# Kernel tuning notes

Measured on AMD Instinct MI355X. Metric: run time of the kernel, lower is better.

The kernel has to match this reference:

```python
import jax, jax.numpy as jnp
import numpy as np

SEQ, BATCH, IN_DIM, HID = 512, 128, 1024, 1024

def setup_inputs() -> dict:
    key = jax.random.key(0)
    k1, k2, k3, k4 = jax.random.split(key, 4)
    scale = 0.02  # keep gate pre-activations in a sane range
    return {
        "inputs": jax.random.normal(k1, (SEQ, BATCH, IN_DIM), dtype=jnp.float32),
        "proj_W": jax.random.normal(k2, (4 * HID, IN_DIM + HID), dtype=jnp.float32) * scale,
        "proj_b": jax.random.normal(k3, (4 * HID,), dtype=jnp.float32) * scale,
        "qgate_W": jax.random.normal(k4, (HID, HID), dtype=jnp.float32) * scale,
    }

def reference(inputs, proj_W, proj_b, qgate_W):
    # inputs: [S, B, I]; proj_W: [4H, I+H]; qgate_W: [H, H]
    S, B, I = inputs.shape
    H = qgate_W.shape[0]
    Wx = proj_W[:, :I]   # [4H, I]
    Wh = proj_W[:, I:]   # [4H, H]
    # Precompute the input part of proj(cat([x, hx])) for all timesteps (same math).
    x_proj = jnp.einsum('sbi,gi->sbg', inputs, Wx) + proj_b  # [S, B, 4H]

    qWt = qgate_W.T
    def qgate(z):
        return jax.nn.sigmoid(z @ qWt)

    def step(carry, xp):
        hx, cx = carry
        gates = xp + hx @ Wh.T  # [B, 4H]
        f_in, i_in, g_in, o_in = jnp.split(gates, 4, axis=-1)
        # mixed/quantum mode: shared quantum gate, then outer nonlinearity (sigmoid of sigmoid, tanh of sigmoid)
        f = jax.nn.sigmoid(qgate(f_in))
        i = jax.nn.sigmoid(qgate(i_in))
        g = jnp.tanh(qgate(g_in))
        o = jax.nn.sigmoid(qgate(o_in))
        cx = f * cx + i * g
        hx = o * jnp.tanh(cx)
        return (hx, cx), hx

    init = (jnp.zeros((B, H), inputs.dtype), jnp.zeros((B, H), inputs.dtype))
    (hx, cx), outs = jax.lax.scan(step, init, x_proj)
    return outs, hx, cx
```

## Files before the change

kernel.cpp:

```cpp
#include <hip/hip_runtime.h>

typedef unsigned short ushort_t;
typedef __attribute__((ext_vector_type(4))) float f32x4;
typedef __attribute__((ext_vector_type(8))) __bf16 bf16x8;

#define SEQ   512
#define BATCH 128
#define HID   1024
#define G4    4096
#define CHUNK 64
#define BH    (BATCH*HID)
#define NBLK  256
#define FLAG_STRIDE 32
#define SCAN_LDS (131072 + 32768)
#define GEMM256_LDS 131072

__device__ __forceinline__ ushort_t f2bf(float f) {
  unsigned u = __float_as_uint(f);
  u += 0x7FFFu + ((u >> 16) & 1u);
  return (ushort_t)(u >> 16);
}
__device__ __forceinline__ float bf2f(ushort_t h) {
  return __uint_as_float(((unsigned)h) << 16);
}
__device__ __forceinline__ float sigm(float x) { return 1.0f / (1.0f + __expf(-x)); }
__device__ __forceinline__ float ftanh(float x) {
  float xc = fminf(fmaxf(x, -15.f), 15.f);
  float t = __expf(2.f * xc);
  return (t - 1.f) / (t + 1.f);
}

__device__ __forceinline__ void lds16(const ushort_t* g, ushort_t* l) {
  __builtin_amdgcn_global_load_lds(
      (const __attribute__((address_space(1))) unsigned int*)g,
      (__attribute__((address_space(3))) unsigned int*)l, 16, 0, 0);
}
__device__ __forceinline__ void lds16c(const ushort_t* g, ushort_t* l) {
  __builtin_amdgcn_global_load_lds(
      (const __attribute__((address_space(1))) unsigned int*)g,
      (__attribute__((address_space(3))) unsigned int*)l, 16, 0, 0x11);
}

__global__ void cast_f32_bf16(const float* __restrict__ in, ushort_t* __restrict__ out, int n4) {
  int i = blockIdx.x * blockDim.x + threadIdx.x;
  if (i < n4) {
    float4 v = ((const float4*)in)[i];
    union { ushort_t u[4]; uint2 v2; } o;
    o.u[0] = f2bf(v.x); o.u[1] = f2bf(v.y); o.u[2] = f2bf(v.z); o.u[3] = f2bf(v.w);
    ((uint2*)out)[i] = o.v2;
  }
}

__global__ __launch_bounds__(256) void transpose_cast(const float* __restrict__ pw, ushort_t* __restrict__ pwt) {
  __shared__ float tile[32][33];
  int bx = blockIdx.x, by = blockIdx.y;
  int tx = threadIdx.x & 31, ty = threadIdx.x >> 5;
  for (int i = 0; i < 32; i += 8)
    tile[ty + i][tx] = pw[(size_t)(by*32 + ty + i)*2048 + bx*32 + tx];
  __syncthreads();
  for (int i = 0; i < 32; i += 8) {
    int r = ty + i;
    pwt[(size_t)(bx*32 + r)*4096 + by*32 + tx] = f2bf(tile[tx][r]);
  }
}

__global__ void bias_fold(const float* __restrict__ qW, const float* __restrict__ pb, float* __restrict__ b2) {
  int r = blockIdx.x;
  int j = r & (HID-1), gb = r & ~(HID-1);
  float s = 0.f;
  for (int k = threadIdx.x; k < HID; k += 64)
    s += qW[(size_t)j*HID + k] * pb[gb + k];
  for (int off = 32; off; off >>= 1) s += __shfl_down(s, off, 64);
  if (threadIdx.x == 0) b2[r] = s;
}

__global__ __launch_bounds__(256) void gemm128(
    const ushort_t* __restrict__ A, int lda, unsigned arow_mask,
    const ushort_t* __restrict__ B, int ldb, unsigned bko_mask,
    const float* __restrict__ bias, ushort_t* __restrict__ C, int ldc, int K)
{
  __shared__ __align__(16) ushort_t Al[128*64];
  __shared__ __align__(16) ushort_t Bl[128*64];
  const int tid = threadIdx.x, wv = tid >> 6, ln = tid & 63;
  const int bn = blockIdx.x, bm = blockIdx.y;
  const int bko = (int)(((unsigned)(bm << 7)) & bko_mask);
  const int m0 = (wv & 1) << 6, n0 = (wv >> 1) << 6;
  f32x4 acc[4][4] = {};
  for (int k0 = 0; k0 < K; k0 += 64) {
    for (int rr = 0; rr < 4; ++rr) {
      int r0 = (rr << 5) + (wv << 3);
      unsigned ga = ((unsigned)((bm << 7) + r0 + (ln >> 3))) & arow_mask;
      lds16(A + (size_t)ga*lda + k0 + ((ln & 7) << 3), &Al[r0 << 6]);
      unsigned gbr = (unsigned)((bn << 7) + r0 + (ln >> 3));
      lds16(B + (size_t)gbr*ldb + bko + k0 + ((ln & 7) << 3), &Bl[r0 << 6]);
    }
    __syncthreads();
    for (int kk = 0; kk < 64; kk += 32) {
      const int lrow = ln & 15, lk = kk + ((ln >> 4) << 3);
      bf16x8 af[4], bfr[4];
      for (int i = 0; i < 4; ++i) af[i]  = *(const bf16x8*)&Al[((m0 + (i << 4) + lrow) << 6) + lk];
      for (int j = 0; j < 4; ++j) bfr[j] = *(const bf16x8*)&Bl[((n0 + (j << 4) + lrow) << 6) + lk];
      for (int i = 0; i < 4; ++i)
        for (int j = 0; j < 4; ++j)
          acc[i][j] = __builtin_amdgcn_mfma_f32_16x16x32_bf16(af[i], bfr[j], acc[i][j], 0, 0, 0);
    }
    __syncthreads();
  }
  for (int i = 0; i < 4; ++i)
    for (int j = 0; j < 4; ++j) {
      int col = (bn << 7) + n0 + (j << 4) + (ln & 15);
      float bv = bias ? bias[col] : 0.f;
      for (int r = 0; r < 4; ++r) {
        int row = (bm << 7) + m0 + (i << 4) + ((ln >> 4) << 2) + r;
        C[(size_t)row*ldc + col] = f2bf(acc[i][j][r] + bv);
      }
    }
}

__global__ __launch_bounds__(512) void gemm256(
    const ushort_t* __restrict__ A, const ushort_t* __restrict__ B,
    const float* __restrict__ bias, ushort_t* __restrict__ C)
{
  extern __shared__ __align__(16) ushort_t lds[];
  ushort_t* LA = lds;
  ushort_t* LB = lds + 32768;
  const int tid = threadIdx.x, wv8 = tid >> 6, ln = tid & 63;
  const int wm = wv8 >> 2, wn = wv8 & 3;
  const int flat = blockIdx.y * gridDim.x + blockIdx.x;
  const int swz  = ((flat & 7) << 6) | (flat >> 3);
  const int bn = swz & 15, bm = swz >> 4;
  const int lr = ln & 15, lg = ln >> 4;

  f32x4 acc[8][4] = {};
  bf16x8 af[4][2], bfr[4][2];

  auto stA = [&](int db, int half, int kt) {
    ushort_t* d = LA + db*16384 + half*8192 + (wv8 << 9);
    const int ce = ((ln & 7) ^ (ln >> 3)) << 3;
    #pragma unroll
    for (int p = 0; p < 2; ++p) {
      int rr = half*128 + p*64 + (wv8 << 3) + (ln >> 3);
      lds16(A + (size_t)(bm*256 + rr)*1024 + kt*64 + ce, d + p*4096);
    }
  };
  auto stB = [&](int db, int half, int kt) {
    ushort_t* d = LB + db*16384 + half*8192 + (wv8 << 9);
    const int ce = ((ln & 7) ^ (ln >> 3)) << 3;
    #pragma unroll
    for (int p = 0; p < 2; ++p) {
      int rr = half*128 + p*64 + (wv8 << 3) + (ln >> 3);
      lds16(B + (size_t)(bn*256 + rr)*2048 + kt*64 + ce, d + p*4096);
    }
  };

#define RD_A(DB, MQ) { _Pragma("unroll") for (int i_ = 0; i_ < 4; ++i_) { \
    const int row_ = ((MQ)*4 + i_)*16 + lr; \
    const ushort_t* b_ = &LA[(DB)*16384 + wm*8192 + row_*64]; \
    af[i_][0] = *(const bf16x8*)&b_[ (lg << 3)       ^ ((lr & 7) << 3)]; \
    af[i_][1] = *(const bf16x8*)&b_[((lg << 3) | 32) ^ ((lr & 7) << 3)]; } }

#define RD_B(DB, NQ) { _Pragma("unroll") for (int j_ = 0; j_ < 2; ++j_) { \
    const int row_ = (wn & 1)*64 + ((NQ)*2 + j_)*16 + lr; \
    const ushort_t* b_ = &LB[(DB)*16384 + (wn >> 1)*8192 + row_*64]; \
    bfr[(NQ)*2 + j_][0] = *(const bf16x8*)&b_[ (lg << 3)       ^ ((lr & 7) << 3)]; \
    bfr[(NQ)*2 + j_][1] = *(const bf16x8*)&b_[((lg << 3) | 32) ^ ((lr & 7) << 3)]; } }

#define QUAD(MQ, NQ) \
  __builtin_amdgcn_s_setprio(1); \
  { _Pragma("unroll") for (int i_ = 0; i_ < 4; ++i_) \
      _Pragma("unroll") for (int j_ = 0; j_ < 2; ++j_) \
        _Pragma("unroll") for (int k_ = 0; k_ < 2; ++k_) \
          acc[(MQ)*4 + i_][(NQ)*2 + j_] = __builtin_amdgcn_mfma_f32_16x16x32_bf16( \
              af[i_][k_], bfr[(NQ)*2 + j_][k_], acc[(MQ)*4 + i_][(NQ)*2 + j_], 0, 0, 0); } \
  __builtin_amdgcn_s_setprio(0);

#define BAR() __builtin_amdgcn_s_barrier()
#define LGK0() do { asm volatile("s_waitcnt lgkmcnt(0)" ::: "memory"); \
                    __builtin_amdgcn_sched_barrier(0); } while (0)
#define VM4() do { asm volatile("s_waitcnt vmcnt(4)" ::: "memory"); \
                   __builtin_amdgcn_sched_barrier(0); } while (0)

  stA(0,0,0); stA(0,1,0); stB(0,0,0); stB(0,1,0); stB(1,0,1); stB(1,1,1);
  asm volatile("s_waitcnt vmcnt(4)" ::: "memory");
  BAR();

  for (int i = 0; i < 8; ++i) {
    const int k1 = 2*i + 1, k2 = 2*i + 2, k3 = 2*i + 3;
    RD_A(0,0); RD_B(0,0); stA(1,0,k1);            BAR(); LGK0(); QUAD(0,0); BAR();
    RD_B(0,1); stA(1,1,k1);                       BAR(); LGK0(); QUAD(0,1); BAR();
    RD_A(0,1); if (k2 < 16) stB(0,0,k2);          BAR(); LGK0(); QUAD(1,0); BAR();
    if (k2 < 16) stB(0,1,k2);                     BAR();         QUAD(1,1); VM4(); BAR();
    RD_A(1,0); RD_B(1,0); if (k2 < 16) stA(0,0,k2); BAR(); LGK0(); QUAD(0,0); BAR();
    RD_B(1,1); if (k2 < 16) stA(0,1,k2);          BAR(); LGK0(); QUAD(0,1); BAR();
    RD_A(1,1); if (k3 < 16) stB(1,0,k3);          BAR(); LGK0(); QUAD(1,0); BAR();
    if (k3 < 16) stB(1,1,k3);                     BAR();         QUAD(1,1); VM4(); BAR();
  }

  const int crow0 = bm*256 + wm*128;
  const int ccol0 = bn*256 + wn*64;
  #pragma unroll
  for (int m = 0; m < 8; ++m)
    #pragma unroll
    for (int n = 0; n < 4; ++n) {
      int col = ccol0 + n*16 + lr;
      float bv = bias[col];
      #pragma unroll
      for (int r = 0; r < 4; ++r) {
        int row = crow0 + m*16 + lg*4 + r;
        C[(size_t)row*4096 + col] = f2bf(acc[m][n][r] + bv);
      }
    }
#undef RD_A
#undef RD_B
#undef QUAD
#undef BAR
#undef LGK0
#undef VM4
}

__global__ __launch_bounds__(256, 1) void qlstm_scan(
    const ushort_t* __restrict__ P,
    const ushort_t* __restrict__ W2,
    ushort_t* __restrict__ hxb,
    float* __restrict__ cxg,
    float* __restrict__ outc,
    int t0,
    unsigned* __restrict__ flags)
{
  extern __shared__ __align__(16) ushort_t lds[];
  ushort_t* Ul = lds;
  ushort_t* Ar = lds + 65536;
  float*    sm = (float*)(lds + 65536);

  const int tid = threadIdx.x, wv = tid >> 6, ln = tid & 63;
  const int rblk = blockIdx.x & 3, cblk = blockIdx.x >> 2;
  unsigned* gflags = flags + (size_t)rblk*64*FLAG_STRIDE;

  for (int ck = 0; ck < 8; ++ck)
    for (int rr = 0; rr < 4; ++rr) {
      int lr = rr*16 + wv*4 + (ln >> 4);
      int grow = ((lr >> 4) << 10) + cblk*16 + (lr & 15);
      int gcol = ck*128 + (((ln & 15) ^ (lr & 7)) << 3);
      lds16(W2 + (size_t)grow*2048 + 1024 + gcol, &Ul[ck*8192 + (rr*16 + wv*4)*128]);
    }

  const int b_loc = tid >> 3;
  const int j0    = (tid & 7) << 1;
  const size_t ci = (size_t)(rblk*32 + b_loc)*1024 + cblk*16 + j0;
  float2 cxr = *(const float2*)&cxg[ci];

  auto stageA = [&](int slot, int k0, const ushort_t* hxR) {
    #pragma unroll
    for (int rr = 0; rr < 2; ++rr) {
      int row = rr*16 + wv*4 + (ln >> 4);
      int gcol = ((ln & 15) ^ (row & 7)) << 3;
      lds16c(hxR + (size_t)(rblk*32 + row)*1024 + k0 + gcol,
             &Ar[slot*4096 + (rr*16 + wv*4)*128]);
    }
  };
  auto load_pv = [&](int tl, float* pv) {
    #pragma unroll
    for (int i = 0; i < 2; ++i)
      #pragma unroll
      for (int r = 0; r < 4; ++r) {
        int bl = i*16 + ((ln >> 4) << 2) + r;
        pv[i*4+r] = bf2f(P[(size_t)(tl*128 + rblk*32 + bl)*4096 + (wv << 10) + cblk*16 + (ln & 15)]);
      }
  };

  float pv[8];
  load_pv(0, pv);

  for (int tl = 0; tl < CHUNK; ++tl) {
    const int t = t0 + tl;
    const ushort_t* hxR = hxb + (size_t)(t % 3)*BH;
    ushort_t*       hxW = hxb + (size_t)((t + 1) % 3)*BH;

    f32x4 acc0 = {}, acc1 = {};
    stageA(0, 0, hxR);
    stageA(1, 128, hxR);
    stageA(2, 256, hxR);

    #define COMPUTE_CK(CK)                                                         \
      {                                                                            \
        const int aslot = (CK) & 3;                                                \
        _Pragma("unroll")                                                          \
        for (int k4 = 0; k4 < 4; ++k4) {                                           \
          int s = k4*4 + (ln >> 4);                                                \
          int ar0 = ln & 15, ar1 = 16 + (ln & 15);                                 \
          int brow = wv*16 + (ln & 15);                                            \
          bf16x8 a0 = *(const bf16x8*)&Ar[aslot*4096 + ar0*128 + ((s ^ (ar0 & 7)) << 3)]; \
          bf16x8 a1 = *(const bf16x8*)&Ar[aslot*4096 + ar1*128 + ((s ^ (ar1 & 7)) << 3)]; \
          bf16x8 bb = *(const bf16x8*)&Ul[(CK)*8192 + brow*128 + ((s ^ (brow & 7)) << 3)]; \
          acc0 = __builtin_amdgcn_mfma_f32_16x16x32_bf16(a0, bb, acc0, 0, 0, 0);   \
          acc1 = __builtin_amdgcn_mfma_f32_16x16x32_bf16(a1, bb, acc1, 0, 0, 0);   \
        }                                                                          \
      }
    #define STEP_CK(CK, WN, DOSTAGE)                                               \
      asm volatile("s_waitcnt vmcnt(" #WN ")" ::: "memory");                       \
      __builtin_amdgcn_s_barrier();                                                \
      if (DOSTAGE) stageA(((CK)+3) & 3, ((CK)+3)*128, hxR);                        \
      COMPUTE_CK(CK)

    STEP_CK(0, 4, 1) STEP_CK(1, 4, 1) STEP_CK(2, 4, 1)
    STEP_CK(3, 4, 1) STEP_CK(4, 4, 1)
    STEP_CK(5, 4, 0) STEP_CK(6, 2, 0) STEP_CK(7, 0, 0)
    #undef STEP_CK
    #undef COMPUTE_CK

    #pragma unroll
    for (int i = 0; i < 2; ++i)
      #pragma unroll
      for (int r = 0; r < 4; ++r) {
        int bl = i*16 + ((ln >> 4) << 2) + r;
        float v = (i ? acc1[r] : acc0[r]) + pv[i*4+r];
        sm[wv*512 + bl*16 + (ln & 15)] = sigm(v);
      }
    __syncthreads();
    float2 h2;
    {
      const float2* sm2 = (const float2*)sm;
      int e = b_loc*8 + (j0 >> 1);
      float2 sF = sm2[0*256 + e], sI = sm2[1*256 + e];
      float2 sG = sm2[2*256 + e], sO = sm2[3*256 + e];
      float f0 = sigm(sF.x), i0 = sigm(sI.x), g0 = ftanh(sG.x), o0 = sigm(sO.x);
      float f1 = sigm(sF.y), i1 = sigm(sI.y), g1 = ftanh(sG.y), o1 = sigm(sO.y);
      float cn0 = f0*cxr.x + i0*g0, cn1 = f1*cxr.y + i1*g1;
      float h0 = o0*ftanh(cn0),     h1 = o1*ftanh(cn1);
      cxr.x = cn0; cxr.y = cn1;
      h2.x = h0; h2.y = h1;
      unsigned hp = (unsigned)f2bf(h0) | ((unsigned)f2bf(h1) << 16);
      __hip_atomic_store((unsigned*)&hxW[ci], hp,
                         __ATOMIC_RELAXED, __HIP_MEMORY_SCOPE_AGENT);
    }

    if (tl != CHUNK - 1) {
      const unsigned gen = (unsigned)(t + 1);
      asm volatile("s_waitcnt vmcnt(0)" ::: "memory");
      __syncthreads();
      if (tid == 0)
        __hip_atomic_store(gflags + (size_t)cblk*FLAG_STRIDE, gen,
                           __ATOMIC_RELAXED, __HIP_MEMORY_SCOPE_AGENT);
      *(float2*)&outc[(size_t)tl*BH + ci] = h2;
      float pvn[8];
      load_pv(tl + 1, pvn);
      if (tid < 64) {
        int it = 0;
        for (;;) {
          unsigned a = __hip_atomic_load(gflags + (size_t)tid*FLAG_STRIDE,
                                         __ATOMIC_RELAXED, __HIP_MEMORY_SCOPE_AGENT);
          if (__all(a >= gen)) break;
          if ((++it & 255) == 0) __builtin_amdgcn_fence(__ATOMIC_ACQUIRE, "agent");
          __builtin_amdgcn_s_sleep(1);
        }
      }
      __syncthreads();
      #pragma unroll
      for (int q = 0; q < 8; ++q) pv[q] = pvn[q];
    } else {
      *(float2*)&outc[(size_t)tl*BH + ci] = h2;
    }
  }
  *(float2*)&cxg[ci] = cxr;
}

extern "C" void kernel_launch(void* const* d_in, const int* in_sizes, int n_in,
                              void* d_out, int out_size, void* d_ws, size_t ws_size,
                              hipStream_t stream) {
  const float* x  = (const float*)d_in[0];
  const float* pW = (const float*)d_in[1];
  const float* pb = (const float*)d_in[2];
  const float* qW = (const float*)d_in[3];
  float* out = (float*)d_out;

  char* w = (char*)d_ws;
  auto carve = [&](size_t bytes) { char* p = w; w += (bytes + 255) & ~(size_t)255; return p; };
  ushort_t* qWbf = (ushort_t*)carve((size_t)HID*HID*2);
  ushort_t* pWt  = (ushort_t*)carve((size_t)2048*4096*2);
  ushort_t* W2   = (ushort_t*)carve((size_t)4096*2048*2);
  float*    b2   = (float*)   carve((size_t)4096*4);
  ushort_t* hxb  = (ushort_t*)carve((size_t)3*BH*2);
  float*    cxws = (float*)   carve((size_t)BH*4);
  unsigned* flags= (unsigned*)carve((size_t)NBLK*FLAG_STRIDE*4);
  ushort_t* xbf  = (ushort_t*)carve((size_t)CHUNK*BATCH*HID*2);
  ushort_t* Pc   = (ushort_t*)carve((size_t)CHUNK*BATCH*G4*2);

  (void)hipFuncSetAttribute((const void*)qlstm_scan,
                            hipFuncAttributeMaxDynamicSharedMemorySize, SCAN_LDS);
  (void)hipFuncSetAttribute((const void*)gemm256,
                            hipFuncAttributeMaxDynamicSharedMemorySize, GEMM256_LDS);

  cast_f32_bf16<<<(HID*HID/4 + 255)/256, 256, 0, stream>>>(qW, qWbf, HID*HID/4);
  transpose_cast<<<dim3(64, 128), 256, 0, stream>>>(pW, pWt);
  bias_fold<<<4096, 64, 0, stream>>>(qW, pb, b2);
  gemm128<<<dim3(16, 32), 256, 0, stream>>>(qWbf, 1024, 1023u, pWt, 4096, ~1023u, nullptr, W2, 2048, 1024);

  hipMemsetAsync(hxb, 0, (size_t)BH*2, stream);
  hipMemsetAsync(cxws, 0, (size_t)BH*4, stream);
  hipMemsetAsync(flags, 0, (size_t)NBLK*FLAG_STRIDE*4, stream);

  for (int c = 0; c < SEQ/CHUNK; ++c) {
    cast_f32_bf16<<<(CHUNK*BATCH*HID/4 + 255)/256, 256, 0, stream>>>(
        x + (size_t)c*CHUNK*BATCH*HID, xbf, CHUNK*BATCH*HID/4);
    gemm256<<<dim3(G4/256, CHUNK*BATCH/256), 512, GEMM256_LDS, stream>>>(
        xbf, W2, b2, Pc);

    const ushort_t* Pa = Pc; const ushort_t* W2a = W2;
    ushort_t* hxa = hxb; float* cxa = cxws;
    float* outa = out + (size_t)c*CHUNK*BH;
    int t0 = c*CHUNK; unsigned* fla = flags;
    void* args[7] = { &Pa, &W2a, &hxa, &cxa, &outa, &t0, &fla };
    hipLaunchCooperativeKernel((const void*)qlstm_scan, dim3(NBLK), dim3(256),
                               args, SCAN_LDS, stream);
  }
  hipMemcpyAsync(out + (size_t)SEQ*BH,      out + (size_t)(SEQ-1)*BH, (size_t)BH*4,
                 hipMemcpyDeviceToDevice, stream);
  hipMemcpyAsync(out + (size_t)SEQ*BH + BH, cxws, (size_t)BH*4,
                 hipMemcpyDeviceToDevice, stream);
}
```

Measured before the change: 2.981 ms.

## Replace flag barrier with generation-tagged hidden-state words polled per chunk

Removes the per-step global flag barrier between scan blocks. Each hidden-state pair is now stored as a 64-bit word tagged with its generation number. Consumers poll the tagged words for each K-chunk directly and spin until all eight words match the expected generation, then unpack them into LDS. This lets a block start computing on early chunks while other producers are still finishing, and it removes the vmcnt drain and flag store. In exchange, hidden-state traffic doubles, LDS staging moves from async global-to-LDS loads to register loads plus LDS writes, and every step spins on many addresses.

```diff
diff --git a/kernel.cpp b/kernel.cpp
--- a/kernel.cpp
+++ b/kernel.cpp
@@ -1,6 +1,7 @@
 #include <hip/hip_runtime.h>
 
 typedef unsigned short ushort_t;
+typedef unsigned long long u64;
 typedef __attribute__((ext_vector_type(4))) float f32x4;
 typedef __attribute__((ext_vector_type(8))) __bf16 bf16x8;
 
@@ -11,9 +12,9 @@
 #define CHUNK 64
 #define BH    (BATCH*HID)
 #define NBLK  256
-#define FLAG_STRIDE 32
 #define SCAN_LDS (131072 + 32768)
 #define GEMM256_LDS 131072
+#define HXATOMS 65536
 
 __device__ __forceinline__ ushort_t f2bf(float f) {
   unsigned u = __float_as_uint(f);
@@ -34,11 +35,6 @@
   __builtin_amdgcn_global_load_lds(
       (const __attribute__((address_space(1))) unsigned int*)g,
       (__attribute__((address_space(3))) unsigned int*)l, 16, 0, 0);
-}
-__device__ __forceinline__ void lds16c(const ushort_t* g, ushort_t* l) {
-  __builtin_amdgcn_global_load_lds(
-      (const __attribute__((address_space(1))) unsigned int*)g,
-      (__attribute__((address_space(3))) unsigned int*)l, 16, 0, 0x11);
 }
 
 __global__ void cast_f32_bf16(const float* __restrict__ in, ushort_t* __restrict__ out, int n4) {
@@ -221,11 +217,10 @@
 __global__ __launch_bounds__(256, 1) void qlstm_scan(
     const ushort_t* __restrict__ P,
     const ushort_t* __restrict__ W2,
-    ushort_t* __restrict__ hxb,
+    u64* __restrict__ hx2,
     float* __restrict__ cxg,
     float* __restrict__ outc,
-    int t0,
-    unsigned* __restrict__ flags)
+    int t0)
 {
   extern __shared__ __align__(16) ushort_t lds[];
   ushort_t* Ul = lds;
@@ -234,30 +229,31 @@
 
   const int tid = threadIdx.x, wv = tid >> 6, ln = tid & 63;
   const int rblk = blockIdx.x & 3, cblk = blockIdx.x >> 2;
-  unsigned* gflags = flags + (size_t)rblk*64*FLAG_STRIDE;
 
   for (int ck = 0; ck < 8; ++ck)
     for (int rr = 0; rr < 4; ++rr) {
-      int lr = rr*16 + wv*4 + (ln >> 4);
-      int grow = ((lr >> 4) << 10) + cblk*16 + (lr & 15);
-      int gcol = ck*128 + (((ln & 15) ^ (lr & 7)) << 3);
+      int lrw = rr*16 + wv*4 + (ln >> 4);
+      int grow = ((lrw >> 4) << 10) + cblk*16 + (lrw & 15);
+      int gcol = ck*128 + (((ln & 15) ^ (lrw & 7)) << 3);
       lds16(W2 + (size_t)grow*2048 + 1024 + gcol, &Ul[ck*8192 + (rr*16 + wv*4)*128]);
     }
 
   const int b_loc = tid >> 3;
   const int j0    = (tid & 7) << 1;
   const size_t ci = (size_t)(rblk*32 + b_loc)*1024 + cblk*16 + j0;
+  const size_t catom = (size_t)(rblk*32 + b_loc)*512 + cblk*8 + (j0 >> 1);
   float2 cxr = *(const float2*)&cxg[ci];
 
-  auto stageA = [&](int slot, int k0, const ushort_t* hxR) {
-    #pragma unroll
-    for (int rr = 0; rr < 2; ++rr) {
-      int row = rr*16 + wv*4 + (ln >> 4);
-      int gcol = ((ln & 15) ^ (row & 7)) << 3;
-      lds16c(hxR + (size_t)(rblk*32 + row)*1024 + k0 + gcol,
-             &Ar[slot*4096 + (rr*16 + wv*4)*128]);
-    }
-  };
+  const int p15 = ln & 15;
+  const int r0l = wv*4 + (ln >> 4);
+  const int r1l = 16 + r0l;
+  const int gc0 = (p15 ^ (r0l & 7)) << 3;
+  const int gc1 = (p15 ^ (r1l & 7)) << 3;
+  const size_t ab0 = (size_t)(rblk*32 + r0l)*512 + (gc0 >> 1);
+  const size_t ab1 = (size_t)(rblk*32 + r1l)*512 + (gc1 >> 1);
+  const int ldo0 = r0l*128 + p15*8;
+  const int ldo1 = r1l*128 + p15*8;
+
   auto load_pv = [&](int tl, float* pv) {
     #pragma unroll
     for (int i = 0; i < 2; ++i)
@@ -268,45 +264,86 @@
       }
   };
 
+#define ISSUE(CK, SRC)                                                           \
+  {                                                                              \
+    const u64* q0_ = (SRC) + ab0 + (CK)*64;                                      \
+    const u64* q1_ = (SRC) + ab1 + (CK)*64;                                      \
+    _Pragma("unroll")                                                            \
+    for (int i_ = 0; i_ < 4; ++i_) {                                             \
+      sv[(CK) % 3][i_]     = __hip_atomic_load(q0_ + i_, __ATOMIC_RELAXED, __HIP_MEMORY_SCOPE_AGENT); \
+      sv[(CK) % 3][4 + i_] = __hip_atomic_load(q1_ + i_, __ATOMIC_RELAXED, __HIP_MEMORY_SCOPE_AGENT); \
+    }                                                                            \
+  }
+
+#define VW(CK)                                                                   \
+  {                                                                              \
+    u64* s8_ = sv[(CK) % 3];                                                     \
+    for (;;) {                                                                   \
+      bool ok_ = ((unsigned)(s8_[0] >> 32) == genr) &&                           \
+                 ((unsigned)(s8_[1] >> 32) == genr) &&                           \
+                 ((unsigned)(s8_[2] >> 32) == genr) &&                           \
+                 ((unsigned)(s8_[3] >> 32) == genr) &&                           \
+                 ((unsigned)(s8_[4] >> 32) == genr) &&                           \
+                 ((unsigned)(s8_[5] >> 32) == genr) &&                           \
+                 ((unsigned)(s8_[6] >> 32) == genr) &&                           \
+                 ((unsigned)(s8_[7] >> 32) == genr);                             \
+      if (__all(ok_)) break;                                                     \
+      const u64* q0_ = hxcur + ab0 + (CK)*64;                                    \
+      const u64* q1_ = hxcur + ab1 + (CK)*64;                                    \
+      _Pragma("unroll")                                                          \
+      for (int i_ = 0; i_ < 4; ++i_) {                                           \
+        s8_[i_]     = __hip_atomic_load(q0_ + i_, __ATOMIC_RELAXED, __HIP_MEMORY_SCOPE_AGENT); \
+        s8_[4 + i_] = __hip_atomic_load(q1_ + i_, __ATOMIC_RELAXED, __HIP_MEMORY_SCOPE_AGENT); \
+      }                                                                          \
+      __builtin_amdgcn_s_sleep(1);                                               \
+    }                                                                            \
+    uint4 w0_, w1_;                                                              \
+    w0_.x = (unsigned)s8_[0]; w0_.y = (unsigned)s8_[1];                          \
+    w0_.z = (unsigned)s8_[2]; w0_.w = (unsigned)s8_[3];                          \
+    w1_.x = (unsigned)s8_[4]; w1_.y = (unsigned)s8_[5];                          \
+    w1_.z = (unsigned)s8_[6]; w1_.w = (unsigned)s8_[7];                          \
+    *(uint4*)&Ar[((CK) & 3)*4096 + ldo0] = w0_;                                  \
+    *(uint4*)&Ar[((CK) & 3)*4096 + ldo1] = w1_;                                  \
+  }
+
+#define COMPUTE_CK(CK)                                                           \
+  {                                                                              \
+    const int aslot = (CK) & 3;                                                  \
+    _Pragma("unroll")                                                            \
+    for (int k4 = 0; k4 < 4; ++k4) {                                             \
+      int s = k4*4 + (ln >> 4);                                                  \
+      int ar0 = ln & 15, ar1 = 16 + (ln & 15);                                   \
+      int brow = wv*16 + (ln & 15);                                              \
+      bf16x8 a0 = *(const bf16x8*)&Ar[aslot*4096 + ar0*128 + ((s ^ (ar0 & 7)) << 3)]; \
+      bf16x8 a1 = *(const bf16x8*)&Ar[aslot*4096 + ar1*128 + ((s ^ (ar1 & 7)) << 3)]; \
+      bf16x8 bb = *(const bf16x8*)&Ul[(CK)*8192 + brow*128 + ((s ^ (brow & 7)) << 3)]; \
+      acc0 = __builtin_amdgcn_mfma_f32_16x16x32_bf16(a0, bb, acc0, 0, 0, 0);     \
+      acc1 = __builtin_amdgcn_mfma_f32_16x16x32_bf16(a1, bb, acc1, 0, 0, 0);     \
+    }                                                                            \
+  }
+
+#define SCK(CK, DOISS)                                                           \
+  VW(CK)                                                                         \
+  if (DOISS) ISSUE((CK)+3, hxcur)                                                \
+  asm volatile("s_waitcnt lgkmcnt(0)" ::: "memory");                             \
+  __builtin_amdgcn_sched_barrier(0);                                             \
+  __builtin_amdgcn_s_barrier();                                                  \
+  COMPUTE_CK(CK)
+
+  u64 sv[3][8];
+  const u64* hxcur = hx2 + (size_t)(t0 % 3)*HXATOMS;
   float pv[8];
   load_pv(0, pv);
+  ISSUE(0, hxcur) ISSUE(1, hxcur) ISSUE(2, hxcur)
 
   for (int tl = 0; tl < CHUNK; ++tl) {
     const int t = t0 + tl;
-    const ushort_t* hxR = hxb + (size_t)(t % 3)*BH;
-    ushort_t*       hxW = hxb + (size_t)((t + 1) % 3)*BH;
+    const unsigned genr = (unsigned)t;
+    u64* hxW2 = hx2 + (size_t)((t + 1) % 3)*HXATOMS;
 
     f32x4 acc0 = {}, acc1 = {};
-    stageA(0, 0, hxR);
-    stageA(1, 128, hxR);
-    stageA(2, 256, hxR);
-
-    #define COMPUTE_CK(CK)                                                         \
-      {                                                                            \
-        const int aslot = (CK) & 3;                                                \
-        _Pragma("unroll")                                                          \
-        for (int k4 = 0; k4 < 4; ++k4) {                                           \
-          int s = k4*4 + (ln >> 4);                                                \
-          int ar0 = ln & 15, ar1 = 16 + (ln & 15);                                 \
-          int brow = wv*16 + (ln & 15);                                            \
-          bf16x8 a0 = *(const bf16x8*)&Ar[aslot*4096 + ar0*128 + ((s ^ (ar0 & 7)) << 3)]; \
-          bf16x8 a1 = *(const bf16x8*)&Ar[aslot*4096 + ar1*128 + ((s ^ (ar1 & 7)) << 3)]; \
-          bf16x8 bb = *(const bf16x8*)&Ul[(CK)*8192 + brow*128 + ((s ^ (brow & 7)) << 3)]; \
-          acc0 = __builtin_amdgcn_mfma_f32_16x16x32_bf16(a0, bb, acc0, 0, 0, 0);   \
-          acc1 = __builtin_amdgcn_mfma_f32_16x16x32_bf16(a1, bb, acc1, 0, 0, 0);   \
-        }                                                                          \
-      }
-    #define STEP_CK(CK, WN, DOSTAGE)                                               \
-      asm volatile("s_waitcnt vmcnt(" #WN ")" ::: "memory");                       \
-      __builtin_amdgcn_s_barrier();                                                \
-      if (DOSTAGE) stageA(((CK)+3) & 3, ((CK)+3)*128, hxR);                        \
-      COMPUTE_CK(CK)
-
-    STEP_CK(0, 4, 1) STEP_CK(1, 4, 1) STEP_CK(2, 4, 1)
-    STEP_CK(3, 4, 1) STEP_CK(4, 4, 1)
-    STEP_CK(5, 4, 0) STEP_CK(6, 2, 0) STEP_CK(7, 0, 0)
-    #undef STEP_CK
-    #undef COMPUTE_CK
+    SCK(0,1) SCK(1,1) SCK(2,1) SCK(3,1) SCK(4,1)
+    SCK(5,0) SCK(6,0) SCK(7,0)
 
     #pragma unroll
     for (int i = 0; i < 2; ++i)
@@ -330,38 +367,27 @@
       cxr.x = cn0; cxr.y = cn1;
       h2.x = h0; h2.y = h1;
       unsigned hp = (unsigned)f2bf(h0) | ((unsigned)f2bf(h1) << 16);
-      __hip_atomic_store((unsigned*)&hxW[ci], hp,
+      u64 pk = (u64)hp | ((u64)(unsigned)(t + 1) << 32);
+      __hip_atomic_store(hxW2 + catom, pk,
                          __ATOMIC_RELAXED, __HIP_MEMORY_SCOPE_AGENT);
     }
+    *(float2*)&outc[(size_t)tl*BH + ci] = h2;
 
     if (tl != CHUNK - 1) {
-      const unsigned gen = (unsigned)(t + 1);
-      asm volatile("s_waitcnt vmcnt(0)" ::: "memory");
-      __syncthreads();
-      if (tid == 0)
-        __hip_atomic_store(gflags + (size_t)cblk*FLAG_STRIDE, gen,
-                           __ATOMIC_RELAXED, __HIP_MEMORY_SCOPE_AGENT);
-      *(float2*)&outc[(size_t)tl*BH + ci] = h2;
       float pvn[8];
       load_pv(tl + 1, pvn);
-      if (tid < 64) {
-        int it = 0;
-        for (;;) {
-          unsigned a = __hip_atomic_load(gflags + (size_t)tid*FLAG_STRIDE,
-                                         __ATOMIC_RELAXED, __HIP_MEMORY_SCOPE_AGENT);
-          if (__all(a >= gen)) break;
-          if ((++it & 255) == 0) __builtin_amdgcn_fence(__ATOMIC_ACQUIRE, "agent");
-          __builtin_amdgcn_s_sleep(1);
-        }
-      }
-      __syncthreads();
+      hxcur = hx2 + (size_t)((t + 1) % 3)*HXATOMS;
+      ISSUE(0, hxcur) ISSUE(1, hxcur) ISSUE(2, hxcur)
       #pragma unroll
       for (int q = 0; q < 8; ++q) pv[q] = pvn[q];
-    } else {
-      *(float2*)&outc[(size_t)tl*BH + ci] = h2;
-    }
+    }
+    __syncthreads();
   }
   *(float2*)&cxg[ci] = cxr;
+#undef ISSUE
+#undef VW
+#undef COMPUTE_CK
+#undef SCK
 }
 
 extern "C" void kernel_launch(void* const* d_in, const int* in_sizes, int n_in,
@@ -379,9 +405,8 @@
   ushort_t* pWt  = (ushort_t*)carve((size_t)2048*4096*2);
   ushort_t* W2   = (ushort_t*)carve((size_t)4096*2048*2);
   float*    b2   = (float*)   carve((size_t)4096*4);
-  ushort_t* hxb  = (ushort_t*)carve((size_t)3*BH*2);
+  u64*      hx2  = (u64*)     carve((size_t)3*HXATOMS*8);
   float*    cxws = (float*)   carve((size_t)BH*4);
-  unsigned* flags= (unsigned*)carve((size_t)NBLK*FLAG_STRIDE*4);
   ushort_t* xbf  = (ushort_t*)carve((size_t)CHUNK*BATCH*HID*2);
   ushort_t* Pc   = (ushort_t*)carve((size_t)CHUNK*BATCH*G4*2);
 
@@ -395,9 +420,8 @@
   bias_fold<<<4096, 64, 0, stream>>>(qW, pb, b2);
   gemm128<<<dim3(16, 32), 256, 0, stream>>>(qWbf, 1024, 1023u, pWt, 4096, ~1023u, nullptr, W2, 2048, 1024);
 
-  hipMemsetAsync(hxb, 0, (size_t)BH*2, stream);
+  hipMemsetAsync(hx2, 0, (size_t)HXATOMS*8, stream);
   hipMemsetAsync(cxws, 0, (size_t)BH*4, stream);
-  hipMemsetAsync(flags, 0, (size_t)NBLK*FLAG_STRIDE*4, stream);
 
   for (int c = 0; c < SEQ/CHUNK; ++c) {
     cast_f32_bf16<<<(CHUNK*BATCH*HID/4 + 255)/256, 256, 0, stream>>>(
@@ -406,10 +430,10 @@
         xbf, W2, b2, Pc);
 
     const ushort_t* Pa = Pc; const ushort_t* W2a = W2;
-    ushort_t* hxa = hxb; float* cxa = cxws;
+    u64* hxa = hx2; float* cxa = cxws;
     float* outa = out + (size_t)c*CHUNK*BH;
-    int t0 = c*CHUNK; unsigned* fla = flags;
-    void* args[7] = { &Pa, &W2a, &hxa, &cxa, &outa, &t0, &fla };
+    int t0 = c*CHUNK;
+    void* args[6] = { &Pa, &W2a, &hxa, &cxa, &outa, &t0 };
     hipLaunchCooperativeKernel((const void*)qlstm_scan, dim3(NBLK), dim3(256),
                                args, SCAN_LDS, stream);
   }
```

New measurement: 6.701 ms. 2.25x slower.
